# Performance work log

Hardware: AMD Instinct MI355X
Metric: run time of the kernel (lower is better)

The kernel has to match this reference:

```python
import jax, jax.numpy as jnp
import numpy as np

VOCAB = 50000
EMBED_DIM = 300
NBINS = 30
B, Q, D = 32, 16, 2048


def setup_inputs() -> dict:
    key = jax.random.key(0)
    ks = jax.random.split(key, 12)
    # ids in [1, VOCAB): id 0 is <PAD>; original code NaNs on pad rows (0/0 norm)
    query = jax.random.randint(ks[0], (B, Q), 1, VOCAB, dtype=jnp.int64 if jax.config.jax_enable_x64 else jnp.int32)
    document = jax.random.randint(ks[1], (B, D), 1, VOCAB, dtype=jnp.int64 if jax.config.jax_enable_x64 else jnp.int32)
    q_idf = jax.random.uniform(ks[2], (B, Q), dtype=jnp.float32)
    emb = jax.random.normal(ks[3], (VOCAB, EMBED_DIM), dtype=jnp.float32) * 0.1
    # ffn: Linear(nbins,5) -> Tanh -> Linear(5,1) -> Tanh -> Linear(1,1) -> Tanh
    W1 = jax.random.normal(ks[4], (NBINS, 5), dtype=jnp.float32) * (1.0 / np.sqrt(NBINS))
    b1 = jnp.zeros((5,), dtype=jnp.float32)
    W2 = jax.random.normal(ks[5], (5, 1), dtype=jnp.float32) * (1.0 / np.sqrt(5.0))
    b2 = jnp.zeros((1,), dtype=jnp.float32)
    W3 = jax.random.normal(ks[6], (1, 1), dtype=jnp.float32)
    b3 = jnp.zeros((1,), dtype=jnp.float32)
    # gate: Linear(embed_dim,1) -> Tanh
    Wg = jax.random.normal(ks[7], (EMBED_DIM, 1), dtype=jnp.float32) * (1.0 / np.sqrt(EMBED_DIM))
    bg = jnp.zeros((1,), dtype=jnp.float32)
    return {"query": query, "document": document, "q_idf": q_idf, "emb": emb,
            "W1": W1, "b1": b1, "W2": W2, "b2": b2, "W3": W3, "b3": b3,
            "Wg": Wg, "bg": bg}


def _histc(x, nbins):
    # torch.histc(x, bins=nbins, min=-1, max=1): values outside [-1,1] dropped,
    # last bin inclusive of max.
    width = 2.0 / nbins
    idx = jnp.clip(jnp.floor((x + 1.0) / width).astype(jnp.int32), 0, nbins - 1)
    valid = ((x >= -1.0) & (x <= 1.0)).astype(x.dtype)
    # (B, Q, D, nbins) one-hot summed over D -> (B, Q, nbins)
    return jnp.sum(jax.nn.one_hot(idx, nbins, dtype=x.dtype) * valid[..., None], axis=2)


def reference(query, document, q_idf, emb, W1, b1, W2, b2, W3, b3, Wg, bg):
    qmask = (query > 0).astype(jnp.float32)          # (B, Q)
    dmask = (document > 0).astype(jnp.float32)       # (B, D)
    qe = emb[query] * qmask[..., None]               # (B, Q, E)
    de = emb[document] * dmask[..., None]            # (B, D, E)
    qn = qe / jnp.linalg.norm(qe, axis=2, keepdims=True)
    dn = de / jnp.linalg.norm(de, axis=2, keepdims=True)
    interaction = jnp.einsum('bqe,bde->bqd', qn, dn)  # cosine sims
    h = jnp.log1p(_histc(interaction, NBINS))         # (B, Q, NBINS)
    z = jnp.tanh(h @ W1 + b1)
    z = jnp.tanh(z @ W2 + b2)
    z = jnp.tanh(z @ W3 + b3)
    z = z.squeeze(-1)                                 # (B, Q)
    g = jnp.tanh(qe @ Wg + bg).squeeze(-1)            # (B, Q)
    exps = jnp.exp(g) * qmask
    g = exps / (exps.sum(axis=1, keepdims=True) + 1e-5)
    return jnp.sum(z * g, axis=1)                     # (B,)
```

## Files before the change

kernel.cpp:

```cpp
#include <hip/hip_runtime.h>

#define B_ 32
#define Q_ 16
#define D_ 2048
#define E_ 300
#define EF4 75
#define NB 30
#define TILE 64
#define TPB (D_ / TILE)

__device__ __forceinline__ float fast_tanh(float x) {
    const float t = __expf(-2.0f * fabsf(x));
    const float r = (1.0f - t) / (1.0f + t);
    return copysignf(r, x);
}
__device__ __forceinline__ float fast_log1p(float x) {
    return __logf(1.0f + x);
}

__global__ __launch_bounds__(256) void drmm_prep(
    const int* __restrict__ query, const float* __restrict__ emb,
    const float* __restrict__ Wg, const float* __restrict__ bg,
    float* __restrict__ qn, float* __restrict__ gbuf, int* __restrict__ hist)
{
    const int b = blockIdx.x, tid = threadIdx.x;
    const int wid = tid >> 6, lane = tid & 63;

    for (int i = b * 256 + tid; i < B_ * Q_ * NB; i += B_ * 256) hist[i] = 0;

    for (int qq = wid; qq < Q_; qq += 4) {
        const int id = query[b * Q_ + qq];
        const float m = (id > 0) ? 1.f : 0.f;
        const float* row = emb + (long long)((id > 0) ? id : 0) * E_;
        float v[5];
        float ss = 0.f, dg = 0.f;
        #pragma unroll
        for (int k = 0; k < 5; ++k) {
            const int e = lane + 64 * k;
            float x = 0.f, w = 0.f;
            if (e < E_) { x = row[e] * m; w = Wg[e]; }
            v[k] = x;
            ss = fmaf(x, x, ss);
            dg = fmaf(x, w, dg);
        }
        #pragma unroll
        for (int off = 32; off > 0; off >>= 1) {
            ss += __shfl_xor(ss, off);
            dg += __shfl_xor(dg, off);
        }
        const float rn = 1.0f / sqrtf(ss);
        #pragma unroll
        for (int k = 0; k < 5; ++k) {
            const int e = lane + 64 * k;
            if (e < E_) qn[((size_t)(b * Q_ + qq)) * E_ + e] = v[k] * rn;
        }
        if (lane == 0) gbuf[b * Q_ + qq] = fast_tanh(dg + bg[0]);
    }
}

__global__ __launch_bounds__(256, 4) void drmm_main(
    const int* __restrict__ doc, const float* __restrict__ emb,
    const float* __restrict__ qn, int* __restrict__ hist)
{
    __shared__ __align__(16) float qs[Q_ * E_];
    __shared__ float part[4][Q_ + 1][TILE];
    __shared__ int   whist[Q_ * NB];

    const int tid = threadIdx.x;
    const int blk = blockIdx.x;
    const int xcd = blk & 7;
    const int j   = blk >> 3;
    const int b   = ((j & 3) << 3) | xcd;
    const int tile = j >> 2;
    const int lane = tid & 63, w = tid >> 6;

    const float4* qb = (const float4*)(qn + (size_t)b * Q_ * E_);
    float4* qs4w = (float4*)qs;
    for (int i = tid; i < Q_ * EF4; i += 256) qs4w[i] = qb[i];
    for (int i = tid; i < Q_ * NB; i += 256) whist[i] = 0;
    __syncthreads();

    const int d = tile * TILE + lane;
    const int id = doc[b * D_ + d];
    const bool rowok = (id > 0);
    const float4* row = (const float4*)(emb + (long long)(rowok ? id : 0) * E_);
    const float4* qs4 = (const float4*)qs;

    const int cbeg = w * 19;
    const int cnt  = (w == 3) ? 18 : 19;

    float acc[Q_];
    #pragma unroll
    for (int q = 0; q < Q_; ++q) acc[q] = 0.f;
    float ss = 0.f;

    #pragma unroll 4
    for (int k = 0; k < cnt; ++k) {
        const int c = cbeg + k;
        const float4 v = row[c];
        ss = fmaf(v.x, v.x, fmaf(v.y, v.y, fmaf(v.z, v.z, fmaf(v.w, v.w, ss))));
        #pragma unroll
        for (int q = 0; q < Q_; ++q) {
            const float4 u = qs4[q * EF4 + c];
            acc[q] = fmaf(v.x, u.x, fmaf(v.y, u.y, fmaf(v.z, u.z, fmaf(v.w, u.w, acc[q]))));
        }
    }

    #pragma unroll
    for (int q = 0; q < Q_; ++q) part[w][q][lane] = acc[q];
    part[w][Q_][lane] = ss;
    __syncthreads();

    const float sst = part[0][Q_][lane] + part[1][Q_][lane]
                    + part[2][Q_][lane] + part[3][Q_][lane];
    const float rn = 1.0f / sqrtf(sst);
    #pragma unroll
    for (int qq = 0; qq < 4; ++qq) {
        const int q = w * 4 + qq;
        const float s = part[0][q][lane] + part[1][q][lane]
                      + part[2][q][lane] + part[3][q][lane];
        const float x = s * rn;
        const float t = (x + 1.0f) * (NB * 0.5f);
        int bin = (int)floorf(t);
        bin = bin < 0 ? 0 : (bin > NB - 1 ? NB - 1 : bin);
        if (rowok && x >= -1.0f && x <= 1.0f)
            atomicAdd(&whist[q * NB + bin], 1);
    }
    __syncthreads();

    for (int i = tid; i < Q_ * NB; i += 256) {
        const int v = whist[i];
        if (v) atomicAdd(&hist[b * Q_ * NB + i], v);
    }
}

__global__ __launch_bounds__(64) void drmm_final(
    const int* __restrict__ hist, const float* __restrict__ gbuf,
    const int* __restrict__ query,
    const float* __restrict__ W1, const float* __restrict__ b1,
    const float* __restrict__ W2, const float* __restrict__ b2,
    const float* __restrict__ W3, const float* __restrict__ b3,
    float* __restrict__ out)
{
    const int b = blockIdx.x, lane = threadIdx.x;
    float z = 0.f, e = 0.f;
    if (lane < Q_) {
        const int* h = hist + (b * Q_ + lane) * NB;
        float pre1[5];
        #pragma unroll
        for (int u = 0; u < 5; ++u) pre1[u] = b1[u];
        #pragma unroll
        for (int k = 0; k < NB; ++k) {
            const float hv = fast_log1p((float)h[k]);
            #pragma unroll
            for (int u = 0; u < 5; ++u) pre1[u] = fmaf(hv, W1[k * 5 + u], pre1[u]);
        }
        float z2 = b2[0];
        #pragma unroll
        for (int u = 0; u < 5; ++u) z2 = fmaf(fast_tanh(pre1[u]), W2[u], z2);
        const float z3 = fmaf(fast_tanh(z2), W3[0], b3[0]);
        z = fast_tanh(z3);
        const int id = query[b * Q_ + lane];
        const float g = gbuf[b * Q_ + lane];
        e = (id > 0) ? __expf(g) : 0.f;
    }
    float ze = z * e, se = e;
    #pragma unroll
    for (int off = 32; off > 0; off >>= 1) {
        ze += __shfl_xor(ze, off);
        se += __shfl_xor(se, off);
    }
    if (lane == 0) out[b] = ze / (se + 1e-5f);
}

extern "C" void kernel_launch(void* const* d_in, const int* in_sizes, int n_in,
                              void* d_out, int out_size, void* d_ws, size_t ws_size,
                              hipStream_t stream)
{
    const int*   query = (const int*)d_in[0];
    const int*   doc   = (const int*)d_in[1];
    const float* emb   = (const float*)d_in[3];
    const float* W1    = (const float*)d_in[4];
    const float* b1    = (const float*)d_in[5];
    const float* W2    = (const float*)d_in[6];
    const float* b2    = (const float*)d_in[7];
    const float* W3    = (const float*)d_in[8];
    const float* b3    = (const float*)d_in[9];
    const float* Wg    = (const float*)d_in[10];
    const float* bg    = (const float*)d_in[11];
    float* out = (float*)d_out;

    char* ws = (char*)d_ws;
    float* qn   = (float*)ws;
    float* gbuf = (float*)(ws + 614400);
    int*   hist = (int*)(ws + 614400 + 2048);

    drmm_prep<<<B_, 256, 0, stream>>>(query, emb, Wg, bg, qn, gbuf, hist);
    drmm_main<<<B_ * TPB, 256, 0, stream>>>(doc, emb, qn, hist);
    drmm_final<<<B_, 64, 0, stream>>>(hist, gbuf, query,
                                      W1, b1, W2, b2, W3, b3, out);
}
```

Before: 49.88 us.

## Process two document rows per thread to reuse shared query loads

Doubles the document tile so each thread computes dot products for two document rows. Each shared-memory query float4 load now feeds FMAs for both rows. All embedding row chunks are loaded into registers up front to raise memory-level parallelism. This halves the block count, lowers the occupancy hint to 2, and raises register pressure with 38 float4s plus 32 accumulators, so the arrays could spill. The histogram step is remapped to 128 rows by two groups of 8 queries, and the pad check re-reads doc ids.

New measurement: 47.79 us. 4.2% less time.

```diff
diff --git a/kernel.cpp b/kernel.cpp
--- a/kernel.cpp
+++ b/kernel.cpp
@@ -6,7 +6,7 @@
 #define E_ 300
 #define EF4 75
 #define NB 30
-#define TILE 64
+#define TILE 128
 #define TPB (D_ / TILE)
 
 __device__ __forceinline__ float fast_tanh(float x) {
@@ -58,7 +58,7 @@
     }
 }
 
-__global__ __launch_bounds__(256, 4) void drmm_main(
+__global__ __launch_bounds__(256, 2) void drmm_main(
     const int* __restrict__ doc, const float* __restrict__ emb,
     const float* __restrict__ qn, int* __restrict__ hist)
 {
@@ -80,51 +80,79 @@
     for (int i = tid; i < Q_ * NB; i += 256) whist[i] = 0;
     __syncthreads();
 
-    const int d = tile * TILE + lane;
-    const int id = doc[b * D_ + d];
-    const bool rowok = (id > 0);
-    const float4* row = (const float4*)(emb + (long long)(rowok ? id : 0) * E_);
+    const int dbase = b * D_ + tile * TILE + lane;
+    const int idA = doc[dbase];
+    const int idB = doc[dbase + 64];
+    const bool okA = (idA > 0), okB = (idB > 0);
+    const int cbeg = w * 19;
+    const bool extra = (w < 3);
+    const float4* rA = ((const float4*)(emb + (long long)(okA ? idA : 0) * E_)) + cbeg;
+    const float4* rB = ((const float4*)(emb + (long long)(okB ? idB : 0) * E_)) + cbeg;
     const float4* qs4 = (const float4*)qs;
 
-    const int cbeg = w * 19;
-    const int cnt  = (w == 3) ? 18 : 19;
-
-    float acc[Q_];
-    #pragma unroll
-    for (int q = 0; q < Q_; ++q) acc[q] = 0.f;
-    float ss = 0.f;
-
-    #pragma unroll 4
-    for (int k = 0; k < cnt; ++k) {
-        const int c = cbeg + k;
-        const float4 v = row[c];
-        ss = fmaf(v.x, v.x, fmaf(v.y, v.y, fmaf(v.z, v.z, fmaf(v.w, v.w, ss))));
+    float4 va[19], vb[19];
+    #pragma unroll
+    for (int k = 0; k < 18; ++k) { va[k] = rA[k]; vb[k] = rB[k]; }
+    if (extra) { va[18] = rA[18]; vb[18] = rB[18]; }
+
+    float accA[Q_], accB[Q_];
+    #pragma unroll
+    for (int q = 0; q < Q_; ++q) { accA[q] = 0.f; accB[q] = 0.f; }
+    float ssA = 0.f, ssB = 0.f;
+
+    #pragma unroll
+    for (int k = 0; k < 18; ++k) {
+        const float4 a = va[k], c = vb[k];
+        ssA = fmaf(a.x, a.x, fmaf(a.y, a.y, fmaf(a.z, a.z, fmaf(a.w, a.w, ssA))));
+        ssB = fmaf(c.x, c.x, fmaf(c.y, c.y, fmaf(c.z, c.z, fmaf(c.w, c.w, ssB))));
         #pragma unroll
         for (int q = 0; q < Q_; ++q) {
-            const float4 u = qs4[q * EF4 + c];
-            acc[q] = fmaf(v.x, u.x, fmaf(v.y, u.y, fmaf(v.z, u.z, fmaf(v.w, u.w, acc[q]))));
-        }
-    }
-
-    #pragma unroll
-    for (int q = 0; q < Q_; ++q) part[w][q][lane] = acc[q];
-    part[w][Q_][lane] = ss;
+            const float4 u = qs4[q * EF4 + cbeg + k];
+            accA[q] = fmaf(a.x, u.x, fmaf(a.y, u.y, fmaf(a.z, u.z, fmaf(a.w, u.w, accA[q]))));
+            accB[q] = fmaf(c.x, u.x, fmaf(c.y, u.y, fmaf(c.z, u.z, fmaf(c.w, u.w, accB[q]))));
+        }
+    }
+    if (extra) {
+        const float4 a = va[18], c = vb[18];
+        ssA = fmaf(a.x, a.x, fmaf(a.y, a.y, fmaf(a.z, a.z, fmaf(a.w, a.w, ssA))));
+        ssB = fmaf(c.x, c.x, fmaf(c.y, c.y, fmaf(c.z, c.z, fmaf(c.w, c.w, ssB))));
+        #pragma unroll
+        for (int q = 0; q < Q_; ++q) {
+            const float4 u = qs4[q * EF4 + cbeg + 18];
+            accA[q] = fmaf(a.x, u.x, fmaf(a.y, u.y, fmaf(a.z, u.z, fmaf(a.w, u.w, accA[q]))));
+            accB[q] = fmaf(c.x, u.x, fmaf(c.y, u.y, fmaf(c.z, u.z, fmaf(c.w, u.w, accB[q]))));
+        }
+    }
+
+    #pragma unroll
+    for (int q = 0; q < Q_; ++q) {
+        part[w][q][lane]      = accA[q];
+        part[w][q][lane + 64] = accB[q];
+    }
+    part[w][Q_][lane]      = ssA;
+    part[w][Q_][lane + 64] = ssB;
     __syncthreads();
 
-    const float sst = part[0][Q_][lane] + part[1][Q_][lane]
-                    + part[2][Q_][lane] + part[3][Q_][lane];
-    const float rn = 1.0f / sqrtf(sst);
-    #pragma unroll
-    for (int qq = 0; qq < 4; ++qq) {
-        const int q = w * 4 + qq;
-        const float s = part[0][q][lane] + part[1][q][lane]
-                      + part[2][q][lane] + part[3][q][lane];
-        const float x = s * rn;
-        const float t = (x + 1.0f) * (NB * 0.5f);
-        int bin = (int)floorf(t);
-        bin = bin < 0 ? 0 : (bin > NB - 1 ? NB - 1 : bin);
-        if (rowok && x >= -1.0f && x <= 1.0f)
-            atomicAdd(&whist[q * NB + bin], 1);
+    {
+        const int r  = tid & 127;
+        const int qh = (tid >> 7) * 8;
+        const float sst = part[0][Q_][r] + part[1][Q_][r]
+                        + part[2][Q_][r] + part[3][Q_][r];
+        const float rn = 1.0f / sqrtf(sst);
+        const bool rok = (r < 64) ? ((doc[b * D_ + tile * TILE + r]) > 0)
+                                  : ((doc[b * D_ + tile * TILE + r]) > 0);
+        #pragma unroll
+        for (int qq = 0; qq < 8; ++qq) {
+            const int q = qh + qq;
+            const float s = part[0][q][r] + part[1][q][r]
+                          + part[2][q][r] + part[3][q][r];
+            const float x = s * rn;
+            const float t = (x + 1.0f) * (NB * 0.5f);
+            int bin = (int)floorf(t);
+            bin = bin < 0 ? 0 : (bin > NB - 1 ? NB - 1 : bin);
+            if (rok && x >= -1.0f && x <= 1.0f)
+                atomicAdd(&whist[q * NB + bin], 1);
+        }
     }
     __syncthreads();
 
```

## Stage document embedding rows in LDS and split query work across waves

Applied to the files above, without the earlier changes.

Each block now processes 32 document rows instead of 64. It first copies their embedding rows into padded shared memory with coalesced float4 loads, where previously each lane gathered its own row strided from global memory. Each wave then handles 4 queries, with lanes split as 32 rows by 2 halves of the embedding dimension. This removes the cross-wave partial-sum buffer in favour of a single shuffle. The change doubles the block count, lowers the occupancy hint to 2, and raises LDS use, which may limit concurrency.

Measured after the change: 70.09 us. +40.5%, slower.

```diff
diff --git a/kernel.cpp b/kernel.cpp
--- a/kernel.cpp
+++ b/kernel.cpp
@@ -6,17 +6,16 @@
 #define E_ 300
 #define EF4 75
 #define NB 30
-#define TILE 64
-#define TPB (D_ / TILE)
+#define TR 32
+#define PITCH 77
+#define TPB (D_ / TR)
 
 __device__ __forceinline__ float fast_tanh(float x) {
     const float t = __expf(-2.0f * fabsf(x));
     const float r = (1.0f - t) / (1.0f + t);
     return copysignf(r, x);
 }
-__device__ __forceinline__ float fast_log1p(float x) {
-    return __logf(1.0f + x);
-}
+__device__ __forceinline__ float fast_log1p(float x) { return __logf(1.0f + x); }
 
 __global__ __launch_bounds__(256) void drmm_prep(
     const int* __restrict__ query, const float* __restrict__ emb,
@@ -58,13 +57,13 @@
     }
 }
 
-__global__ __launch_bounds__(256, 4) void drmm_main(
+__global__ __launch_bounds__(256, 2) void drmm_main(
     const int* __restrict__ doc, const float* __restrict__ emb,
     const float* __restrict__ qn, int* __restrict__ hist)
 {
-    __shared__ __align__(16) float qs[Q_ * E_];
-    __shared__ float part[4][Q_ + 1][TILE];
-    __shared__ int   whist[Q_ * NB];
+    __shared__ __align__(16) float4 ds[TR * PITCH];
+    __shared__ __align__(16) float4 qs4[Q_ * EF4];
+    __shared__ int whist[Q_ * NB];
 
     const int tid = threadIdx.x;
     const int blk = blockIdx.x;
@@ -75,56 +74,69 @@
     const int lane = tid & 63, w = tid >> 6;
 
     const float4* qb = (const float4*)(qn + (size_t)b * Q_ * E_);
-    float4* qs4w = (float4*)qs;
-    for (int i = tid; i < Q_ * EF4; i += 256) qs4w[i] = qb[i];
+    for (int i = tid; i < Q_ * EF4; i += 256) qs4[i] = qb[i];
     for (int i = tid; i < Q_ * NB; i += 256) whist[i] = 0;
+
+    const int rowbase = b * D_ + tile * TR;
+    #pragma unroll 2
+    for (int i = 0; i < 8; ++i) {
+        const int r = w * 8 + i;
+        const int rid = doc[rowbase + r];
+        const float4* g4 = (const float4*)(emb + (long long)(rid > 0 ? rid : 0) * E_);
+        ds[r * PITCH + lane] = g4[lane];
+        if (lane < EF4 - 64) ds[r * PITCH + 64 + lane] = g4[64 + lane];
+    }
     __syncthreads();
 
-    const int d = tile * TILE + lane;
-    const int id = doc[b * D_ + d];
-    const bool rowok = (id > 0);
-    const float4* row = (const float4*)(emb + (long long)(rowok ? id : 0) * E_);
-    const float4* qs4 = (const float4*)qs;
-
-    const int cbeg = w * 19;
-    const int cnt  = (w == 3) ? 18 : 19;
-
-    float acc[Q_];
-    #pragma unroll
-    for (int q = 0; q < Q_; ++q) acc[q] = 0.f;
-    float ss = 0.f;
-
-    #pragma unroll 4
-    for (int k = 0; k < cnt; ++k) {
-        const int c = cbeg + k;
-        const float4 v = row[c];
-        ss = fmaf(v.x, v.x, fmaf(v.y, v.y, fmaf(v.z, v.z, fmaf(v.w, v.w, ss))));
-        #pragma unroll
-        for (int q = 0; q < Q_; ++q) {
-            const float4 u = qs4[q * EF4 + c];
-            acc[q] = fmaf(v.x, u.x, fmaf(v.y, u.y, fmaf(v.z, u.z, fmaf(v.w, u.w, acc[q]))));
-        }
-    }
-
-    #pragma unroll
-    for (int q = 0; q < Q_; ++q) part[w][q][lane] = acc[q];
-    part[w][Q_][lane] = ss;
-    __syncthreads();
-
-    const float sst = part[0][Q_][lane] + part[1][Q_][lane]
-                    + part[2][Q_][lane] + part[3][Q_][lane];
-    const float rn = 1.0f / sqrtf(sst);
-    #pragma unroll
-    for (int qq = 0; qq < 4; ++qq) {
-        const int q = w * 4 + qq;
-        const float s = part[0][q][lane] + part[1][q][lane]
-                      + part[2][q][lane] + part[3][q][lane];
-        const float x = s * rn;
-        const float t = (x + 1.0f) * (NB * 0.5f);
-        int bin = (int)floorf(t);
-        bin = bin < 0 ? 0 : (bin > NB - 1 ? NB - 1 : bin);
-        if (rowok && x >= -1.0f && x <= 1.0f)
-            atomicAdd(&whist[q * NB + bin], 1);
+    const int r = lane & 31, h = lane >> 5;
+    const int rid = doc[rowbase + r];
+    const float4* drow = ds + r * PITCH;
+    const float4* qA = qs4 + (w * 4 + 0) * EF4;
+    const float4* qB = qs4 + (w * 4 + 1) * EF4;
+    const float4* qC = qs4 + (w * 4 + 2) * EF4;
+    const float4* qD = qs4 + (w * 4 + 3) * EF4;
+
+    float a0 = 0.f, a1 = 0.f, a2 = 0.f, a3 = 0.f, ss = 0.f;
+    for (int kk = 0; kk < 37; ++kk) {
+        const int k = 2 * kk + h;
+        const float4 d = drow[k];
+        ss = fmaf(d.x, d.x, fmaf(d.y, d.y, fmaf(d.z, d.z, fmaf(d.w, d.w, ss))));
+        float4 u;
+        u = qA[k]; a0 = fmaf(d.x,u.x, fmaf(d.y,u.y, fmaf(d.z,u.z, fmaf(d.w,u.w, a0))));
+        u = qB[k]; a1 = fmaf(d.x,u.x, fmaf(d.y,u.y, fmaf(d.z,u.z, fmaf(d.w,u.w, a1))));
+        u = qC[k]; a2 = fmaf(d.x,u.x, fmaf(d.y,u.y, fmaf(d.z,u.z, fmaf(d.w,u.w, a2))));
+        u = qD[k]; a3 = fmaf(d.x,u.x, fmaf(d.y,u.y, fmaf(d.z,u.z, fmaf(d.w,u.w, a3))));
+    }
+    if (h == 0) {
+        const float4 d = drow[74];
+        ss = fmaf(d.x, d.x, fmaf(d.y, d.y, fmaf(d.z, d.z, fmaf(d.w, d.w, ss))));
+        float4 u;
+        u = qA[74]; a0 = fmaf(d.x,u.x, fmaf(d.y,u.y, fmaf(d.z,u.z, fmaf(d.w,u.w, a0))));
+        u = qB[74]; a1 = fmaf(d.x,u.x, fmaf(d.y,u.y, fmaf(d.z,u.z, fmaf(d.w,u.w, a1))));
+        u = qC[74]; a2 = fmaf(d.x,u.x, fmaf(d.y,u.y, fmaf(d.z,u.z, fmaf(d.w,u.w, a2))));
+        u = qD[74]; a3 = fmaf(d.x,u.x, fmaf(d.y,u.y, fmaf(d.z,u.z, fmaf(d.w,u.w, a3))));
+    }
+
+    a0 += __shfl_xor(a0, 32);
+    a1 += __shfl_xor(a1, 32);
+    a2 += __shfl_xor(a2, 32);
+    a3 += __shfl_xor(a3, 32);
+    ss += __shfl_xor(ss, 32);
+
+    if (h == 0) {
+        const float rn = 1.0f / sqrtf(ss);
+        const bool rok = (rid > 0);
+        const int qbase = w * 4;
+        float xs[4] = {a0 * rn, a1 * rn, a2 * rn, a3 * rn};
+        #pragma unroll
+        for (int qq = 0; qq < 4; ++qq) {
+            const float x = xs[qq];
+            const float t = (x + 1.0f) * (NB * 0.5f);
+            int bin = (int)floorf(t);
+            bin = bin < 0 ? 0 : (bin > NB - 1 ? NB - 1 : bin);
+            if (rok && x >= -1.0f && x <= 1.0f)
+                atomicAdd(&whist[(qbase + qq) * NB + bin], 1);
+        }
     }
     __syncthreads();
 
```
